# Performance work log

Measured on AMD Instinct MI355X. Metric: run time of the kernel, lower is better.

## Reference

```python
import jax, jax.numpy as jnp
import numpy as np

N_ROW = 50000
N_COL = 50000
E = 600000
D = 128
NEG_SLOPE = 0.01  # torch LeakyReLU default


def _leaky(x):
    return jnp.where(x >= 0, x, NEG_SLOPE * x)


def _mlp(x, W1, b1, W2, b2):
    # (Linear -> LeakyReLU) x2, matching nn.Sequential in Conv_layer
    h = _leaky(x @ W1 + b1)
    return _leaky(h @ W2 + b2)


def setup_inputs() -> dict:
    key = jax.random.key(0)
    ks = jax.random.split(key, 16)
    inp = {
        "feat_row": jax.random.normal(ks[0], (N_ROW, D), jnp.float32),
        "feat_col": jax.random.normal(ks[1], (N_COL, D), jnp.float32),
        "src_c2r": jax.random.randint(ks[2], (E,), 0, N_COL, jnp.int32),
        "dst_c2r": jax.random.randint(ks[3], (E,), 0, N_ROW, jnp.int32),
        "w_c2r": jax.random.uniform(ks[4], (E,), jnp.float32),
        "src_r2c": jax.random.randint(ks[5], (E,), 0, N_ROW, jnp.int32),
        "dst_r2c": jax.random.randint(ks[6], (E,), 0, N_COL, jnp.int32),
        "w_r2c": jax.random.uniform(ks[7], (E,), jnp.float32),
        "W1_c2r": jax.random.normal(ks[8], (D, D), jnp.float32) / np.sqrt(D),
        "b1_c2r": jax.random.normal(ks[9], (D,), jnp.float32) * 0.01,
        "W2_c2r": jax.random.normal(ks[10], (D, D), jnp.float32) / np.sqrt(D),
        "b2_c2r": jax.random.normal(ks[11], (D,), jnp.float32) * 0.01,
        "W1_r2c": jax.random.normal(ks[12], (D, D), jnp.float32) / np.sqrt(D),
        "b1_r2c": jax.random.normal(ks[13], (D,), jnp.float32) * 0.01,
        "W2_r2c": jax.random.normal(ks[14], (D, D), jnp.float32) / np.sqrt(D),
        "b2_r2c": jax.random.normal(ks[15], (D,), jnp.float32) * 0.01,
        "eps_c2r": jnp.zeros((), jnp.float32),  # DGL GINConv init_eps=0
        "eps_r2c": jnp.zeros((), jnp.float32),
    }
    return inp


def reference(feat_row, feat_col, src_c2r, dst_c2r, w_c2r, src_r2c, dst_r2c, w_r2c,
              W1_c2r, b1_c2r, W2_c2r, b2_c2r, W1_r2c, b1_r2c, W2_r2c, b2_r2c,
              eps_c2r, eps_r2c):
    # col -> row GINConv (edge-weighted sum aggregation)
    msg = feat_col[src_c2r] * w_c2r[:, None]                       # [E, D]
    agg_row = jax.ops.segment_sum(msg, dst_c2r, num_segments=N_ROW)
    h_row = _mlp((1.0 + eps_c2r) * feat_row + agg_row, W1_c2r, b1_c2r, W2_c2r, b2_c2r)
    # row -> col GINConv using updated row features
    msg2 = h_row[src_r2c] * w_r2c[:, None]                         # [E, D]
    agg_col = jax.ops.segment_sum(msg2, dst_r2c, num_segments=N_COL)
    h_col = _mlp((1.0 + eps_r2c) * feat_col + agg_col, W1_r2c, b1_r2c, W2_r2c, b2_r2c)
    # residual (use_residual=True): add pre-conv embeddings
    return h_row + feat_row, h_col + feat_col
```

## Files before the change

### kernel.cpp

```cpp
#include <hip/hip_runtime.h>
#include <hip/hip_bf16.h>

#define NROW 50000
#define NCOL 50000
#define DDIM 128
#define CAP  32

typedef __bf16 bf16_t;
typedef __bf16 bf16x2 __attribute__((ext_vector_type(2)));
typedef __bf16 bf16x8 __attribute__((ext_vector_type(8)));
typedef float  f32x4  __attribute__((ext_vector_type(4)));

__device__ __forceinline__ float lrelu(float v) { return v >= 0.f ? v : 0.01f * v; }

__device__ __forceinline__ float ldf(const void* p, size_t i, bool f) {
    return f ? ((const float*)p)[i] : (float)((const bf16_t*)p)[i];
}

__device__ __forceinline__ bool dtf(const int* flags, int fi) {
    return (fi == -1) ? true : (fi == -2) ? false : (flags[fi] != 0);
}

struct TensorTab { const void* p[18]; int n[18]; };

// ... 19 lines not shown
        unsigned low = w & 0xffffu;
        if (low) {
            int e = (int)((low >> 7) & 0xffu);
            if (e >= 90 && e <= 141) atomicAdd(&vb, 1);
            else                     atomicAdd(&vf, 1);
        }
    }
    __syncthreads();
    if (tid == 0) flags[t] = (isFloatArr && vf > vb) ? 1 : 0;
}

__device__ __forceinline__ void fill_edges(
    int e, const int* __restrict__ dst, const int* __restrict__ srcArr,
    const void* __restrict__ wArr, int nE, int* __restrict__ counts,
    int2* __restrict__ slots2, int* __restrict__ ovCnt,
    int* __restrict__ ovList, bool fW)
{
    if (e >= nE) return;
    int d = dst[e];
    int pos = atomicAdd(&counts[d], 1);
    if (pos < CAP) {
        int2 pk;
        pk.x = srcArr[e];
        pk.y = __float_as_int(ldf(wArr, e, fW));
        slots2[(size_t)d * CAP + pos] = pk;
    } else {
        int k = atomicAdd(ovCnt, 1);
        ovList[k] = e;
    }
}

struct WPtrs { const void* W[4]; int fi[4]; };

__global__ __launch_bounds__(256) void prep_fill(
    WPtrs P, const int* __restrict__ flags, __bf16* __restrict__ wfp,
    const void* __restrict__ feat, __bf16* __restrict__ cbuf, int n8,
    int fiFeat, int cblocks,
    const int* __restrict__ f_dst, const int* __restrict__ f_src,
    const void* __restrict__ f_w, int f_nE, int* __restrict__ f_counts,
    int2* __restrict__ f_slots2, int* __restrict__ f_ovCnt,
    int* __restrict__ f_ovList, int f_fiW)
{
    const int b = blockIdx.x;
    const int tid = threadIdx.x;
    if (b < cblocks) {
        int i = b * 256 + tid;
        if (i >= n8) return;
        const bool f = dtf(flags, fiFeat);
        bf16x8 v;
        if (f) {
            f32x4 a = ((const f32x4*)feat)[i * 2];
            f32x4 c = ((const f32x4*)feat)[i * 2 + 1];
#pragma unroll
            for (int j = 0; j < 4; ++j) { v[j] = (__bf16)a[j]; v[j + 4] = (__bf16)c[j]; }
        } else {
            v = ((const bf16x8*)feat)[i];
        }
        ((bf16x8*)cbuf)[i] = v;
    } else if (b < cblocks + 32) {
        int slot = (b - cblocks) * 256 + tid;
        if (slot >= 4 * 2048) return;
        int m = slot >> 11, sIdx = slot & 2047;
        bool f = flags[P.fi[m]] != 0;
        int l = sIdx & 63, combo = sIdx >> 6;
        int ct = combo >> 2, kk = combo & 3;
        int col  = ct * 16 + (l & 15);
        int krow = kk * 32 + (l >> 4) * 8;
        bf16x8 v;
#pragma unroll
        for (int j = 0; j < 8; ++j)
            v[j] = (__bf16)ldf(P.W[m], (size_t)(krow + j) * DDIM + col, f);
        ((bf16x8*)wfp)[slot] = v;
    } else {
        int e = (b - cblocks - 32) * 256 + tid;
        fill_edges(e, f_dst, f_src, f_w, f_nE, f_counts, f_slots2,
                   f_ovCnt, f_ovList, dtf(flags, f_fiW));
    }
}

__global__ __launch_bounds__(256) void segsum_scan(
    const __bf16* __restrict__ gsrc, const int* __restrict__ counts,
    const int2* __restrict__ slots2, float* __restrict__ agg, int nRows,
    const int* __restrict__ srcArr, const int* __restrict__ dstArr,
    const void* __restrict__ wArr, const int* __restrict__ ovList,
    const int* __restrict__ ovCount, const int* __restrict__ flags, int fiW)
{
    int row = blockIdx.x * 4 + (threadIdx.x >> 6);
    if (row >= nRows) return;
    int lane = threadIdx.x & 63;

    int cntRaw = counts[row];
    int cnt = cntRaw > CAP ? CAP : cntRaw;

    int sr = 0; float wv = 0.f;
    if (lane < cnt) {
        int2 pk = slots2[(size_t)row * CAP + lane];
        sr = pk.x;
        wv = __int_as_float(pk.y);
    }

    float2* ap = (float2*)(agg + (size_t)row * DDIM) + lane;
    float2 acc0 = {0.f, 0.f}, acc1 = {0.f, 0.f};

    const bf16x2* fb = (const bf16x2*)gsrc;
    int i = 0;
// ... 159 lines not shown
    for (int cp = 0; cp < 2; ++cp) {
        const int ct = cp ? ct1 : ct0;
        f32x4 acc = {0.f, 0.f, 0.f, 0.f};
#pragma unroll
        for (int kk = 0; kk < 4; ++kk)
            acc = __builtin_amdgcn_mfma_f32_16x16x32_bf16(
                a2[kk], cp ? wfb[kk] : wfa[kk], acc, 0, 0, 0);
        float bias = cp ? b2b : b2a;
#pragma unroll
        for (int gg = 0; gg < 4; ++gg) {
            int row = rowBase + quad * 4 + gg;
            float v = lrelu(acc[gg] + bias);
            if (HOUT)
                At[(quad * 4 + gg) * 136 + ct * 16 + r] = (__bf16)v;
            if (row < N) {
                int col = ct * 16 + r;
                if (RESIDUAL) v += ldf(feat, (size_t)row * DDIM + col, fF);
                out[(size_t)row * DDIM + col] = v;
            }
        }
    }

    if (HOUT) {
        __syncthreads();
        int row = tid >> 4;
        int k0  = (tid & 15) * 8;
        int g   = rowBase + row;
        if (g < N)
            *(bf16x8*)&hout[(size_t)g * DDIM + k0] =
                *(const bf16x8*)&At[row * 136 + k0];
    }
}

__global__ __launch_bounds__(256) void prep_all(
    WPtrs P, const int* __restrict__ flags, __bf16* __restrict__ wfp,
    const void* __restrict__ feat, __bf16* __restrict__ cbuf, int n8, int fiFeat,
    int* __restrict__ zc, int zn, int cblocks, int zblocks)
{
    const int b = blockIdx.x;
    const int tid = threadIdx.x;
    if (b < cblocks) {
        int i = b * 256 + tid;
        if (i >= n8) return;
        const bool f = dtf(flags, fiFeat);
        bf16x8 v;
        if (f) {
            f32x4 a = ((const f32x4*)feat)[i * 2];
            f32x4 c = ((const f32x4*)feat)[i * 2 + 1];
#pragma unroll
            for (int j = 0; j < 4; ++j) { v[j] = (__bf16)a[j]; v[j + 4] = (__bf16)c[j]; }
        } else {
            v = ((const bf16x8*)feat)[i];
        }
        ((bf16x8*)cbuf)[i] = v;
    } else if (b < cblocks + zblocks) {
        int i = (b - cblocks) * 256 + tid;
        if (i < zn) zc[i] = 0;
    } else {
        int slot = (b - cblocks - zblocks) * 256 + tid;
        if (slot >= 4 * 2048) return;
        int m = slot >> 11, sIdx = slot & 2047;
        bool f = flags[P.fi[m]] != 0;
        int l = sIdx & 63, combo = sIdx >> 6;
        int ct = combo >> 2, kk = combo & 3;
        int col  = ct * 16 + (l & 15);
        int krow = kk * 32 + (l >> 4) * 8;
        bf16x8 v;
#pragma unroll
        for (int j = 0; j < 8; ++j)
            v[j] = (__bf16)ldf(P.W[m], (size_t)(krow + j) * DDIM + col, f);
        ((bf16x8*)wfp)[slot] = v;
    }
}

__global__ __launch_bounds__(256) void fill_slots_packed(
    const int* __restrict__ dst, const int* __restrict__ srcArr,
    const void* __restrict__ wArr, int nE, int* __restrict__ counts,
    int2* __restrict__ slots2, int* __restrict__ ovCount,
    int* __restrict__ ovList, float* __restrict__ agg,
    const int* __restrict__ flags, int fiW)
{
    int e = blockIdx.x * 256 + threadIdx.x;
    if (e >= nE) return;
    const bool fW = dtf(flags, fiW);
    int d = dst[e];
    int pos = atomicAdd(&counts[d], 1);
    if (pos < CAP) {
        int2 pk;
        pk.x = srcArr[e];
        pk.y = __float_as_int(ldf(wArr, e, fW));
        slots2[(size_t)d * CAP + pos] = pk;
    } else {
        if (pos == CAP) {
            f32x4 z = {0.f, 0.f, 0.f, 0.f};
            f32x4* rp = (f32x4*)(agg + (size_t)d * DDIM);
#pragma unroll 4
            for (int c = 0; c < DDIM / 4; ++c) rp[c] = z;
        }
        int k = atomicAdd(ovCount, 1);
        ovList[k] = e;
    }
}

__global__ __launch_bounds__(256) void segsum_ov(
    const __bf16* __restrict__ gsrc, const int* __restrict__ counts,
    const int2* __restrict__ slots2, float* __restrict__ agg, int nRows,
    const int* __restrict__ srcArr, const int* __restrict__ dstArr,
    const void* __restrict__ wArr, const int* __restrict__ ovList,
    const int* __restrict__ ovCount, const int* __restrict__ flags, int fiW,
    int gblocks)
{
    const int tid  = threadIdx.x;
    const int lane = tid & 63;

    if ((int)blockIdx.x >= gblocks) {
        const bool fW = dtf(flags, fiW);
        const int nOv = *ovCount;
        const int wv_ = tid >> 6;
        const int nWaves = 64 * 4;
        for (int k = (blockIdx.x - gblocks) * 4 + wv_; k < nOv; k += nWaves) {
            int e = ovList[k];
            int s = srcArr[e], d = dstArr[e];
            float wf = ldf(wArr, e, fW);
            bf16x2 v = ((const bf16x2*)gsrc)[(size_t)s * 64 + lane];
            float* ap = agg + (size_t)d * DDIM + lane * 2;
            unsafeAtomicAdd(ap + 0, (float)v[0] * wf);
            unsafeAtomicAdd(ap + 1, (float)v[1] * wf);
        }
        return;
    }

    int row = blockIdx.x * 4 + (tid >> 6);
    if (row >= nRows) return;

    int cntRaw = counts[row];
    int cnt = cntRaw > CAP ? CAP : cntRaw;

    int sr = 0; float wv = 0.f;
    if (lane < cnt) {
        int2 pk = slots2[(size_t)row * CAP + lane];
        sr = pk.x;
        wv = __int_as_float(pk.y);
    }

    float2* ap = (float2*)(agg + (size_t)row * DDIM) + lane;
    float2 acc0 = {0.f, 0.f}, acc1 = {0.f, 0.f};

    const bf16x2* fb = (const bf16x2*)gsrc;
    int i = 0;
    for (; i + 4 <= cnt; i += 4) {
        int   a0 = __shfl(sr, i),     a1 = __shfl(sr, i + 1);
        int   a2 = __shfl(sr, i + 2), a3 = __shfl(sr, i + 3);
        float w0 = __shfl(wv, i),     w1 = __shfl(wv, i + 1);
        float w2 = __shfl(wv, i + 2), w3 = __shfl(wv, i + 3);
        bf16x2 v0 = fb[(size_t)a0 * 64 + lane];
        bf16x2 v1 = fb[(size_t)a1 * 64 + lane];
        bf16x2 v2 = fb[(size_t)a2 * 64 + lane];
        bf16x2 v3 = fb[(size_t)a3 * 64 + lane];
        acc0.x += (float)v0[0] * w0; acc0.y += (float)v0[1] * w0;
        acc1.x += (float)v1[0] * w1; acc1.y += (float)v1[1] * w1;
        acc0.x += (float)v2[0] * w2; acc0.y += (float)v2[1] * w2;
        acc1.x += (float)v3[0] * w3; acc1.y += (float)v3[1] * w3;
    }
    for (; i < cnt; ++i) {
        int   a0 = __shfl(sr, i);
        float w0 = __shfl(wv, i);
        bf16x2 v0 = fb[(size_t)a0 * 64 + lane];
        acc0.x += (float)v0[0] * w0; acc0.y += (float)v0[1] * w0;
    }
    acc0.x += acc1.x; acc0.y += acc1.y;
    if (cntRaw > CAP) {
        unsafeAtomicAdd(&ap->x, acc0.x);
        unsafeAtomicAdd(&ap->y, acc0.y);
    } else {
        *ap = acc0;
    }
}

template <bool RESIDUAL, bool HOUT>
__global__ __launch_bounds__(256) void mlp_reg(
    const void* __restrict__ feat, const float* __restrict__ agg,
    const void* __restrict__ b1, const void* __restrict__ b2,
    const void* __restrict__ epsp, float* __restrict__ out, int N,
    const int* __restrict__ flags, int fiFeat, int fiB1, int fiB2, int fiEps,
    const __bf16* __restrict__ pW1, const __bf16* __restrict__ pW2,
    __bf16* __restrict__ hout, int* __restrict__ zc, int zn)
{
    __shared__ alignas(16) __bf16 h1t[64 * 136];

    const int tid  = threadIdx.x;
    if (zc) {
        int gi = blockIdx.x * 256 + tid;
        if (gi < zn) zc[gi] = 0;
    }

    const bool fF  = flags[fiFeat] != 0;
    const bool fB1 = flags[fiB1] != 0;
    const bool fB2 = flags[fiB2] != 0;
    const bool fE  = flags[fiEps] != 0;

    const int lane = tid & 63;
    const int wave = tid >> 6;
    const int quad = lane >> 4;
    const int r    = lane & 15;
    const int rowBase = blockIdx.x * 64 + wave * 16;

    const bf16x8* pw1v = (const bf16x8*)pW1;
    bf16x8 w1f[32];
#pragma unroll
    for (int i = 0; i < 32; ++i) w1f[i] = pw1v[i * 64 + lane];

    float bias1[8];
#pragma unroll
    for (int ct = 0; ct < 8; ++ct) bias1[ct] = ldf(b1, ct * 16 + r, fB1);
    const float eps1 = 1.f + ldf(epsp, 0, fE);

    bf16x8 a[4];
    {
        int rowA = rowBase + r;
        if (rowA < N) {
            size_t fb = (size_t)rowA * DDIM + quad * 8;
            const f32x4* gp = (const f32x4*)(agg + fb);
            if (fF) {
                const f32x4* fp = (const f32x4*)((const float*)feat + fb);
#pragma unroll
                for (int kk = 0; kk < 4; ++kk) {
                    f32x4 f0 = fp[kk * 8], f1 = fp[kk * 8 + 1];
                    f32x4 g0 = gp[kk * 8], g1 = gp[kk * 8 + 1];
                    bf16x8 av;
#pragma unroll
                    for (int j = 0; j < 4; ++j) {
                        av[j]     = (__bf16)(f0[j] * eps1 + g0[j]);
                        av[j + 4] = (__bf16)(f1[j] * eps1 + g1[j]);
                    }
                    a[kk] = av;
                }
            } else {
                const bf16x8* fp = (const bf16x8*)((const bf16_t*)feat + fb);
#pragma unroll
                for (int kk = 0; kk < 4; ++kk) {
                    bf16x8 fv = fp[kk * 4];
                    f32x4 g0 = gp[kk * 8], g1 = gp[kk * 8 + 1];
                    bf16x8 av;
#pragma unroll
                    for (int j = 0; j < 4; ++j) {
                        av[j]     = (__bf16)((float)fv[j]     * eps1 + g0[j]);
                        av[j + 4] = (__bf16)((float)fv[j + 4] * eps1 + g1[j]);
                    }
                    a[kk] = av;
                }
            }
        } else {
#pragma unroll
            for (int kk = 0; kk < 4; ++kk)
#pragma unroll
                for (int j = 0; j < 8; ++j) a[kk][j] = (__bf16)0.f;
        }
    }

#pragma unroll
    for (int ct = 0; ct < 8; ++ct) {
        f32x4 acc = {0.f, 0.f, 0.f, 0.f};
#pragma unroll
        for (int kk = 0; kk < 4; ++kk)
            acc = __builtin_amdgcn_mfma_f32_16x16x32_bf16(
                a[kk], w1f[ct * 4 + kk], acc, 0, 0, 0);
#pragma unroll
        for (int gg = 0; gg < 4; ++gg)
            h1t[(wave * 16 + quad * 4 + gg) * 136 + ct * 16 + r] =
                (__bf16)lrelu(acc[gg] + bias1[ct]);
    }

    bf16x8 a2[4];
#pragma unroll
    for (int kk = 0; kk < 4; ++kk)
        a2[kk] = *(const bf16x8*)&h1t[(wave * 16 + r) * 136 + kk * 32 + quad * 8];

    const bf16x8* pw2v = (const bf16x8*)pW2;
    bf16x8 w2f[32];
#pragma unroll
    for (int i = 0; i < 32; ++i) w2f[i] = pw2v[i * 64 + lane];
    float bias2[8];
#pragma unroll
    for (int ct = 0; ct < 8; ++ct) bias2[ct] = ldf(b2, ct * 16 + r, fB2);

#pragma unroll
    for (int ct = 0; ct < 8; ++ct) {
        f32x4 acc = {0.f, 0.f, 0.f, 0.f};
#pragma unroll
        for (int kk = 0; kk < 4; ++kk)
            acc = __builtin_amdgcn_mfma_f32_16x16x32_bf16(
                a2[kk], w2f[ct * 4 + kk], acc, 0, 0, 0);
#pragma unroll
        for (int gg = 0; gg < 4; ++gg) {
            int row = rowBase + quad * 4 + gg;
            float v = lrelu(acc[gg] + bias2[ct]);
            if (HOUT)
                h1t[(wave * 16 + quad * 4 + gg) * 136 + ct * 16 + r] = (__bf16)v;
            if (row < N) {
                int col = ct * 16 + r;
                if (RESIDUAL) v += ldf(feat, (size_t)row * DDIM + col, fF);
                out[(size_t)row * DDIM + col] = v;
            }
        }
    }

    if (HOUT) {
        __syncthreads();
        const int blockBase = blockIdx.x * 64;
#pragma unroll
        for (int c = 0; c < 4; ++c) {
            int chunk = tid + c * 256;
            int row = chunk >> 4;
            int k   = (chunk & 15) * 8;
            if (blockBase + row < N) {
                bf16x8 v = *(const bf16x8*)&h1t[row * 136 + k];
                *(bf16x8*)&hout[(size_t)(blockBase + row) * DDIM + k] = v;
            }
        }
    }
}

__global__ __launch_bounds__(256) void scatter_any(
    const void* __restrict__ feat, const int* __restrict__ src,
    const int* __restrict__ dst, const void* __restrict__ w,
    float* __restrict__ agg, int nE,
    const int* __restrict__ flags, int fiFeat, int fiW)
{
    const bool fF = dtf(flags, fiFeat);
    const bool fW = dtf(flags, fiW);
    int g = blockIdx.x * 256 + threadIdx.x;
    int e = g >> 5;
    if (e >= nE) return;
    int c = (g & 31) << 2;
    int s = src[e], d = dst[e];
    float wf = ldf(w, e, fW);
    size_t base = (size_t)s * DDIM + c;
    float* ap = agg + (size_t)d * DDIM + c;
    unsafeAtomicAdd(ap + 0, ldf(feat, base + 0, fF) * wf);
    unsafeAtomicAdd(ap + 1, ldf(feat, base + 1, fF) * wf);
    unsafeAtomicAdd(ap + 2, ldf(feat, base + 2, fF) * wf);
    unsafeAtomicAdd(ap + 3, ldf(feat, base + 3, fF) * wf);
}

__global__ __launch_bounds__(256) void residual_add(
    float* __restrict__ out, const void* __restrict__ feat, int n4,
    const int* __restrict__ flags, int fiFeat)
{
    const bool fF = flags[fiFeat] != 0;
    int i = blockIdx.x * 256 + threadIdx.x;
    if (i >= n4) return;
    f32x4 o = ((const f32x4*)out)[i];
    f32x4 r;
#pragma unroll
    for (int j = 0; j < 4; ++j) r[j] = o[j] + ldf(feat, (size_t)i * 4 + j, fF);
// ... 119 lines not shown
    for (int ct = 0; ct < 8; ++ct) {
        f32x4 acc = {0.f, 0.f, 0.f, 0.f};
#pragma unroll
        for (int kk = 0; kk < 4; ++kk)
            acc = __builtin_amdgcn_mfma_f32_16x16x32_bf16(
                a2[kk], wv[(ct * 4 + kk) * 64 + lane], acc, 0, 0, 0);
        float bias = ldf(b2, ct * 16 + r, fB2);
#pragma unroll
        for (int gg = 0; gg < 4; ++gg) {
            int row = rowBase + quad * 4 + gg;
            if (row < N) {
                int col = ct * 16 + r;
                float v = lrelu(acc[gg] + bias);
                if (RESIDUAL) v += ldf(feat, (size_t)row * DDIM + col, fF);
                out[(size_t)row * DDIM + col] = v;
            }
        }
    }
}

extern "C" void kernel_launch(void* const* d_in, const int* in_sizes, int n_in,
                              void* d_out, int out_size, void* d_ws, size_t ws_size,
                              hipStream_t stream)
{
    const int* src_c2r = (const int*)d_in[2];
    const int* dst_c2r = (const int*)d_in[3];
    const int* src_r2c = (const int*)d_in[5];
    const int* dst_r2c = (const int*)d_in[6];
    const int nE = in_sizes[2];

    char* wsb = (char*)d_ws;
    int*    flags  = (int*)wsb;
    __bf16* wfprep = (__bf16*)(wsb + 128);
    int*    countsA = (int*)(wsb + 128 + 131072);
    int*    ovCntA  = countsA + NROW;
    int*    countsB = countsA + NROW + 8;
    int*    ovCntB  = countsA + 2 * NROW + 8;
    size_t  ofsA2   = 128 + 131072 + ((size_t)2 * NROW + 16) * 4;
    ofsA2 = (ofsA2 + 15) & ~(size_t)15;
    int2*   slots2A2  = (int2*)(wsb + ofsA2);
    size_t  ofsOvA2   = ofsA2 + (size_t)NROW * CAP * 8;
    int*    ovListA2  = (int*)(wsb + ofsOvA2);
    int*    ovListB2  = ovListA2 + nE;
    size_t  ofsCbA2   = (ofsOvA2 + (size_t)nE * 8 + 15) & ~(size_t)15;
    __bf16* cbufA2    = (__bf16*)(wsb + ofsCbA2);
    const size_t NEED_A2 = ofsCbA2 + (size_t)NROW * DDIM * 2;

    int*    counts = (int*)(wsb + 128 + 131072);
    int*    ovCnt  = counts + NROW;
    size_t  ofs    = 128 + 131072 + ((size_t)NROW + 8) * 4;
    ofs = (ofs + 15) & ~(size_t)15;
    int2*   slots2 = (int2*)(wsb + ofs);
    size_t  ofsOvA = ofs + (size_t)NROW * CAP * 8;
    int*    ovListA = (int*)(wsb + ofsOvA);
    size_t  ofsCb  = (ofsOvA + (size_t)nE * 4 + 15) & ~(size_t)15;
    __bf16* cbuf   = (__bf16*)(wsb + ofsCb);
    const size_t NEED_A = ofsCb + (size_t)NROW * DDIM * 2;

    const bool tierA2 = ws_size >= NEED_A2;
    const bool tierA  = ws_size >= NEED_A;

    TensorTab T;
    for (int i = 0; i < 18; ++i) { T.p[i] = d_in[i]; T.n[i] = in_sizes[i]; }

    float* out_row = (float*)d_out;
    float* out_col = out_row + (size_t)NROW * DDIM;
    const size_t aggBytes = (size_t)NROW * DDIM * sizeof(float);

    const int eblocks  = (nE + 255) / 256;
    const int sblocks  = (nE * 32 + 255) / 256;
    const int mblocksR = (NROW + 63) / 64;
    const int mblocksC = (NCOL + 63) / 64;
    const int csR      = (NROW + 15) / 16;
    const int csC      = (NCOL + 15) / 16;
    const int gblocksR = (NROW + 3) / 4;
    const int gblocksC = (NCOL + 3) / 4;
    const int cblocks  = (NCOL * DDIM / 8 + 255) / 256;

    WPtrs P;
    P.W[0] = d_in[8];  P.fi[0] = 8;
    P.W[1] = d_in[10]; P.fi[1] = 10;
    P.W[2] = d_in[12]; P.fi[2] = 12;
    P.W[3] = d_in[14]; P.fi[3] = 14;

    if (tierA2) {
        const int zn2 = 2 * NROW + 16;
        const int zb2 = (zn2 + 255) / 256;
        detect_zero<<<18 + zb2, 256, 0, stream>>>(T, flags, countsA, zn2);
        prep_fill<<<cblocks + 32 + eblocks, 256, 0, stream>>>(
            P, flags, wfprep, d_in[1], cbufA2, NCOL * DDIM / 8, 1, cblocks,
            dst_c2r, src_c2r, d_in[4], nE, countsA, slots2A2, ovCntA,
            ovListA2, 4);
        segsum_scan<<<gblocksR, 256, 0, stream>>>(cbufA2, countsA, slots2A2,
            out_col, NROW, src_c2r, dst_c2r, d_in[4], ovListA2, ovCntA,
            flags, 4);
        mlp_cs<true, true><<<csR + eblocks, 256, 0, stream>>>(
            d_in[0], out_col, d_in[9], d_in[11], d_in[16],
            out_row, NROW, flags, 0, 9, 11, 16,
            wfprep + 0 * 16384, wfprep + 1 * 16384, cbufA2,
            csR, dst_r2c, src_r2c, d_in[7], nE, countsB, slots2A2,
            ovCntB, ovListB2, 7);
        segsum_scan<<<gblocksC, 256, 0, stream>>>(cbufA2, countsB, slots2A2,
            out_col, NCOL, src_r2c, dst_r2c, d_in[7], ovListB2, ovCntB,
            flags, 7);
        mlp_cs<true, false><<<csC, 256, 0, stream>>>(
            d_in[1], out_col, d_in[13], d_in[15], d_in[17],
            out_col, NCOL, flags, 1, 13, 15, 17,
            wfprep + 2 * 16384, wfprep + 3 * 16384, nullptr,
            csC, nullptr, nullptr, nullptr, 0, nullptr, nullptr,
            nullptr, nullptr, 0);
    } else if (tierA) {
        const int zblocks = ((NROW + 8) + 255) / 256;
        const int zn      = NROW + 8;
        detect_zero<<<18, 256, 0, stream>>>(T, flags, nullptr, 0);
        prep_all<<<cblocks + zblocks + 32, 256, 0, stream>>>(
            P, flags, wfprep, d_in[1], cbuf, NCOL * DDIM / 8, 1,
            counts, zn, cblocks, zblocks);
        fill_slots_packed<<<eblocks, 256, 0, stream>>>(dst_c2r, src_c2r,
            d_in[4], nE, counts, slots2, ovCnt, ovListA, out_col, flags, 4);
        segsum_ov<<<gblocksR + 64, 256, 0, stream>>>(cbuf, counts, slots2,
            out_col, NROW, src_c2r, dst_c2r, d_in[4], ovListA, ovCnt,
            flags, 4, gblocksR);
        mlp_reg<true, true><<<mblocksR, 256, 0, stream>>>(
            d_in[0], out_col, d_in[9], d_in[11], d_in[16],
            out_row, NROW, flags, 0, 9, 11, 16,
            wfprep + 0 * 16384, wfprep + 1 * 16384, cbuf, counts, zn);
        fill_slots_packed<<<eblocks, 256, 0, stream>>>(dst_r2c, src_r2c,
            d_in[7], nE, counts, slots2, ovCnt, ovListA, out_col, flags, 7);
        segsum_ov<<<gblocksC + 64, 256, 0, stream>>>(cbuf, counts, slots2,
            out_col, NCOL, src_r2c, dst_r2c, d_in[7], ovListA, ovCnt,
            flags, 7, gblocksC);
        mlp_reg<true, false><<<mblocksC, 256, 0, stream>>>(
            d_in[1], out_col, d_in[13], d_in[15], d_in[17],
            out_col, NCOL, flags, 1, 13, 15, 17,
            wfprep + 2 * 16384, wfprep + 3 * 16384, nullptr, nullptr, 0);
    } else {
        detect_zero<<<18, 256, 0, stream>>>(T, flags, nullptr, 0);
        hipMemsetAsync(out_col, 0, aggBytes, stream);
        scatter_any<<<sblocks, 256, 0, stream>>>(d_in[1], src_c2r, dst_c2r,
            d_in[4], out_col, nE, flags, 1, 4);
        mlp_kernel<false><<<mblocksR, 256, 0, stream>>>(
            d_in[0], out_col, d_in[8], d_in[9], d_in[10], d_in[11], d_in[16],
            out_row, NROW, flags, 0, 8, 9, 10, 11, 16);

        hipMemsetAsync(out_col, 0, aggBytes, stream);
        scatter_any<<<sblocks, 256, 0, stream>>>(out_row, src_r2c, dst_r2c,
            d_in[7], out_col, nE, flags, -1, 7);
        residual_add<<<(NROW * DDIM / 4 + 255) / 256, 256, 0, stream>>>(
            out_row, d_in[0], NROW * DDIM / 4, flags, 0);
        mlp_kernel<true><<<mblocksC, 256, 0, stream>>>(
            d_in[1], out_col, d_in[12], d_in[13], d_in[14], d_in[15], d_in[17],
            out_col, NCOL, flags, 1, 12, 13, 14, 15, 17);
    }
}
```

Before: 309.5 us.

## Fuse gather-sum into MLP kernel and interleave edge-fill with compute blocks

```diff
diff --git a/kernel.cpp b/kernel.cpp
--- a/kernel.cpp
+++ b/kernel.cpp
@@ -75,6 +75,276 @@
 
 struct WPtrs { const void* W[4]; int fi[4]; };
 
+__device__ __forceinline__ void prep_one(WPtrs P, const int* flags,
+                                         __bf16* wfp, int slot)
+{
+    if (slot >= 4 * 2048) return;
+    int m = slot >> 11, sIdx = slot & 2047;
+    bool f = flags[P.fi[m]] != 0;
+    int l = sIdx & 63, combo = sIdx >> 6;
+    int ct = combo >> 2, kk = combo & 3;
+    int col  = ct * 16 + (l & 15);
+    int krow = kk * 32 + (l >> 4) * 8;
+    bf16x8 v;
+#pragma unroll
+    for (int j = 0; j < 8; ++j)
+        v[j] = (__bf16)ldf(P.W[m], (size_t)(krow + j) * DDIM + col, f);
+    ((bf16x8*)wfp)[slot] = v;
+}
+
+__device__ __forceinline__ void convert_one(const void* __restrict__ feat,
+                                            __bf16* __restrict__ cbuf,
+                                            int i, int n8, bool f)
+{
+    if (i >= n8) return;
+    bf16x8 v;
+    if (f) {
+        f32x4 a = ((const f32x4*)feat)[i * 2];
+        f32x4 c = ((const f32x4*)feat)[i * 2 + 1];
+#pragma unroll
+        for (int j = 0; j < 4; ++j) { v[j] = (__bf16)a[j]; v[j + 4] = (__bf16)c[j]; }
+    } else {
+        v = ((const bf16x8*)feat)[i];
+    }
+    ((bf16x8*)cbuf)[i] = v;
+}
+
+__global__ __launch_bounds__(256) void prep_fill_i(
+    WPtrs P, const int* __restrict__ flags, __bf16* __restrict__ wfp,
+    const void* __restrict__ feat, __bf16* __restrict__ cbuf, int n8,
+    int fiFeat, int cb, int eb, int K7,
+    const int* __restrict__ f_dst, const int* __restrict__ f_src,
+    const void* __restrict__ f_w, int f_nE, int* __restrict__ f_counts,
+    int2* __restrict__ f_slots2, int* __restrict__ f_ovCnt,
+    int* __restrict__ f_ovList, int f_fiW)
+{
+    const int g = blockIdx.x;
+    const int tid = threadIdx.x;
+    if (g >= K7) {
+        prep_one(P, flags, wfp, (g - K7) * 256 + tid);
+        return;
+    }
+    int grp = g / 7, rem = g % 7;
+    if (rem < 4) {
+        int b = grp * 4 + rem;
+        if (b >= cb) return;
+        convert_one(feat, cbuf, b * 256 + tid, n8, dtf(flags, fiFeat));
+    } else {
+        int b = grp * 3 + (rem - 4);
+        if (b >= eb) return;
+        fill_edges(b * 256 + tid, f_dst, f_src, f_w, f_nE, f_counts,
+                   f_slots2, f_ovCnt, f_ovList, dtf(flags, f_fiW));
+    }
+}
+
+template <bool RESIDUAL, bool HOUT>
+__global__ __launch_bounds__(256) void mlp_fused(
+    const __bf16* __restrict__ gsrc, const int* __restrict__ counts,
+    const int2* __restrict__ slots2, const int* __restrict__ srcArr,
+    const int* __restrict__ dstArr, const void* __restrict__ wArr,
+    const int* __restrict__ ovList, const int* __restrict__ ovCount, int fiW,
+    const void* __restrict__ feat, const void* __restrict__ b1,
+    const void* __restrict__ b2, const void* __restrict__ epsp,
+    float* __restrict__ out, int N, const int* __restrict__ flags,
+    int fiFeat, int fiB1, int fiB2, int fiEps,
+    const __bf16* __restrict__ pW1, const __bf16* __restrict__ pW2,
+    __bf16* __restrict__ hout,
+    int mlpBlocks, int fillBlocks,
+    const int* __restrict__ f_dst, const int* __restrict__ f_src,
+    const void* __restrict__ f_w, int f_nE, int* __restrict__ f_counts,
+    int2* __restrict__ f_slots2, int* __restrict__ f_ovCnt,
+    int* __restrict__ f_ovList, int f_fiW)
+{
+    __shared__ alignas(16) __bf16 At[16 * 136];
+    __shared__ alignas(16) __bf16 H1[16 * 136];
+
+    const int tid = threadIdx.x;
+    int bid;
+    if (f_dst) {
+        int grp = (int)blockIdx.x / 7, rem = (int)blockIdx.x % 7;
+        if (rem >= 4) {
+            int b = grp * 3 + (rem - 4);
+            if (b < fillBlocks)
+                fill_edges(b * 256 + tid, f_dst, f_src, f_w, f_nE, f_counts,
+                           f_slots2, f_ovCnt, f_ovList, dtf(flags, f_fiW));
+            return;
+        }
+        bid = grp * 4 + rem;
+        if (bid >= mlpBlocks) return;
+    } else {
+        bid = blockIdx.x;
+        if (bid >= mlpBlocks) return;
+    }
+
+    const bool fF  = flags[fiFeat] != 0;
+    const bool fB1 = flags[fiB1] != 0;
+    const bool fB2 = flags[fiB2] != 0;
+    const bool fE  = flags[fiEps] != 0;
+
+    const int lane = tid & 63;
+    const int wave = tid >> 6;
+    const int quad = lane >> 4;
+    const int r    = lane & 15;
+    const int rowBase = bid * 16;
+    const float eps1 = 1.f + ldf(epsp, 0, fE);
+
+    {
+        const bf16x2* fb = (const bf16x2*)gsrc;
+        for (int j = 0; j < 4; ++j) {
+            int lrow = wave * 4 + j;
+            int row  = rowBase + lrow;
+            bf16x2 o;
+            if (row < N) {
+                int cntRaw = counts[row];
+                int cnt = cntRaw > CAP ? CAP : cntRaw;
+                int sr = 0; float wv = 0.f;
+                if (lane < cnt) {
+                    int2 pk = slots2[(size_t)row * CAP + lane];
+                    sr = pk.x;
+                    wv = __int_as_float(pk.y);
+                }
+                float2 acc0 = {0.f, 0.f}, acc1 = {0.f, 0.f};
+                int i = 0;
+                for (; i + 4 <= cnt; i += 4) {
+                    int   a0 = __shfl(sr, i),     a1 = __shfl(sr, i + 1);
+                    int   a2 = __shfl(sr, i + 2), a3 = __shfl(sr, i + 3);
+                    float w0 = __shfl(wv, i),     w1 = __shfl(wv, i + 1);
+                    float w2 = __shfl(wv, i + 2), w3 = __shfl(wv, i + 3);
+                    bf16x2 v0 = fb[(size_t)a0 * 64 + lane];
+                    bf16x2 v1 = fb[(size_t)a1 * 64 + lane];
+                    bf16x2 v2 = fb[(size_t)a2 * 64 + lane];
+                    bf16x2 v3 = fb[(size_t)a3 * 64 + lane];
+                    acc0.x += (float)v0[0] * w0; acc0.y += (float)v0[1] * w0;
+                    acc1.x += (float)v1[0] * w1; acc1.y += (float)v1[1] * w1;
+                    acc0.x += (float)v2[0] * w2; acc0.y += (float)v2[1] * w2;
+                    acc1.x += (float)v3[0] * w3; acc1.y += (float)v3[1] * w3;
+                }
+                for (; i < cnt; ++i) {
+                    int   a0 = __shfl(sr, i);
+                    float w0 = __shfl(wv, i);
+                    bf16x2 v0 = fb[(size_t)a0 * 64 + lane];
+                    acc0.x += (float)v0[0] * w0; acc0.y += (float)v0[1] * w0;
+                }
+                if (cntRaw > CAP) {
+                    const bool fW = dtf(flags, fiW);
+                    int nOv = *ovCount;
+                    for (int k = 0; k < nOv; ++k) {
+                        int e = ovList[k];
+                        if (dstArr[e] == row) {
+                            int s = srcArr[e];
+                            float wf = ldf(wArr, e, fW);
+                            bf16x2 v = fb[(size_t)s * 64 + lane];
+                            acc0.x += (float)v[0] * wf;
+                            acc0.y += (float)v[1] * wf;
+                        }
+                    }
+                }
+                float ax = acc0.x + acc1.x, ay = acc0.y + acc1.y;
+                float f0, f1;
+                if (fF) {
+                    float2 fv = ((const float2*)((const float*)feat +
+                                 (size_t)row * DDIM))[lane];
+                    f0 = fv.x; f1 = fv.y;
+                } else {
+                    bf16x2 fv = ((const bf16x2*)((const bf16_t*)feat +
+                                 (size_t)row * DDIM))[lane];
+                    f0 = (float)fv[0]; f1 = (float)fv[1];
+                }
+                o[0] = (__bf16)(f0 * eps1 + ax);
+                o[1] = (__bf16)(f1 * eps1 + ay);
+            } else {
+                o[0] = (__bf16)0.f; o[1] = (__bf16)0.f;
+            }
+            *(bf16x2*)&At[lrow * 136 + lane * 2] = o;
+        }
+    }
+    __syncthreads();
+
+    bf16x8 a[4];
+#pragma unroll
+    for (int kk = 0; kk < 4; ++kk)
+        a[kk] = *(const bf16x8*)&At[r * 136 + kk * 32 + quad * 8];
+
+    const int ct0 = wave * 2, ct1 = ct0 + 1;
+
+    const bf16x8* pw1v = (const bf16x8*)pW1;
+    bf16x8 wfa[4], wfb[4];
+#pragma unroll
+    for (int kk = 0; kk < 4; ++kk) {
+        wfa[kk] = pw1v[(ct0 * 4 + kk) * 64 + lane];
+        wfb[kk] = pw1v[(ct1 * 4 + kk) * 64 + lane];
+    }
+    float b1a = ldf(b1, ct0 * 16 + r, fB1);
+    float b1b = ldf(b1, ct1 * 16 + r, fB1);
+
+    {
+        f32x4 acc = {0.f, 0.f, 0.f, 0.f};
+#pragma unroll
+        for (int kk = 0; kk < 4; ++kk)
+            acc = __builtin_amdgcn_mfma_f32_16x16x32_bf16(a[kk], wfa[kk], acc, 0, 0, 0);
+#pragma unroll
+        for (int gg = 0; gg < 4; ++gg)
+            H1[(quad * 4 + gg) * 136 + ct0 * 16 + r] = (__bf16)lrelu(acc[gg] + b1a);
+    }
+    {
+        f32x4 acc = {0.f, 0.f, 0.f, 0.f};
+#pragma unroll
+        for (int kk = 0; kk < 4; ++kk)
+            acc = __builtin_amdgcn_mfma_f32_16x16x32_bf16(a[kk], wfb[kk], acc, 0, 0, 0);
+#pragma unroll
+        for (int gg = 0; gg < 4; ++gg)
+            H1[(quad * 4 + gg) * 136 + ct1 * 16 + r] = (__bf16)lrelu(acc[gg] + b1b);
+    }
+    __syncthreads();
+
+    bf16x8 a2[4];
+#pragma unroll
+    for (int kk = 0; kk < 4; ++kk)
+        a2[kk] = *(const bf16x8*)&H1[r * 136 + kk * 32 + quad * 8];
+
+    const bf16x8* pw2v = (const bf16x8*)pW2;
+#pragma unroll
+    for (int kk = 0; kk < 4; ++kk) {
+        wfa[kk] = pw2v[(ct0 * 4 + kk) * 64 + lane];
+        wfb[kk] = pw2v[(ct1 * 4 + kk) * 64 + lane];
+    }
+    float b2a = ldf(b2, ct0 * 16 + r, fB2);
+    float b2b = ldf(b2, ct1 * 16 + r, fB2);
+
+#pragma unroll
+    for (int cp = 0; cp < 2; ++cp) {
+        const int ct = cp ? ct1 : ct0;
+        f32x4 acc = {0.f, 0.f, 0.f, 0.f};
+#pragma unroll
+        for (int kk = 0; kk < 4; ++kk)
+            acc = __builtin_amdgcn_mfma_f32_16x16x32_bf16(
+                a2[kk], cp ? wfb[kk] : wfa[kk], acc, 0, 0, 0);
+        float bias = cp ? b2b : b2a;
+#pragma unroll
+        for (int gg = 0; gg < 4; ++gg) {
+            int row = rowBase + quad * 4 + gg;
+            float v = lrelu(acc[gg] + bias);
+            if (HOUT)
+                At[(quad * 4 + gg) * 136 + ct * 16 + r] = (__bf16)v;
+            if (row < N) {
+                int col = ct * 16 + r;
+                if (RESIDUAL) v += ldf(feat, (size_t)row * DDIM + col, fF);
+                out[(size_t)row * DDIM + col] = v;
+            }
+        }
+    }
+
+    if (HOUT) {
+        __syncthreads();
+        int row = tid >> 4;
+        int k0  = (tid & 15) * 8;
+        int g   = rowBase + row;
+        if (g < N)
+            *(bf16x8*)&hout[(size_t)g * DDIM + k0] =
+                *(const bf16x8*)&At[row * 136 + k0];
+    }
+}
+
 __global__ __launch_bounds__(256) void prep_fill(
     WPtrs P, const int* __restrict__ flags, __bf16* __restrict__ wfp,
     const void* __restrict__ feat, __bf16* __restrict__ cbuf, int n8,
@@ -87,33 +357,9 @@
     const int b = blockIdx.x;
     const int tid = threadIdx.x;
     if (b < cblocks) {
-        int i = b * 256 + tid;
-        if (i >= n8) return;
-        const bool f = dtf(flags, fiFeat);
-        bf16x8 v;
-        if (f) {
-            f32x4 a = ((const f32x4*)feat)[i * 2];
-            f32x4 c = ((const f32x4*)feat)[i * 2 + 1];
-#pragma unroll
-            for (int j = 0; j < 4; ++j) { v[j] = (__bf16)a[j]; v[j + 4] = (__bf16)c[j]; }
-        } else {
-            v = ((const bf16x8*)feat)[i];
-        }
-        ((bf16x8*)cbuf)[i] = v;
+        convert_one(feat, cbuf, b * 256 + tid, n8, dtf(flags, fiFeat));
     } else if (b < cblocks + 32) {
-        int slot = (b - cblocks) * 256 + tid;
-        if (slot >= 4 * 2048) return;
-        int m = slot >> 11, sIdx = slot & 2047;
-        bool f = flags[P.fi[m]] != 0;
-        int l = sIdx & 63, combo = sIdx >> 6;
-        int ct = combo >> 2, kk = combo & 3;
-        int col  = ct * 16 + (l & 15);
-        int krow = kk * 32 + (l >> 4) * 8;
-        bf16x8 v;
-#pragma unroll
-        for (int j = 0; j < 8; ++j)
-            v[j] = (__bf16)ldf(P.W[m], (size_t)(krow + j) * DDIM + col, f);
-        ((bf16x8*)wfp)[slot] = v;
+        prep_one(P, flags, wfp, (b - cblocks) * 256 + tid);
     } else {
         int e = (b - cblocks - 32) * 256 + tid;
         fill_edges(e, f_dst, f_src, f_w, f_nE, f_counts, f_slots2,
@@ -339,295 +585,6 @@
     }
 }
 
-__global__ __launch_bounds__(256) void prep_all(
-    WPtrs P, const int* __restrict__ flags, __bf16* __restrict__ wfp,
-    const void* __restrict__ feat, __bf16* __restrict__ cbuf, int n8, int fiFeat,
-    int* __restrict__ zc, int zn, int cblocks, int zblocks)
-{
-    const int b = blockIdx.x;
-    const int tid = threadIdx.x;
-    if (b < cblocks) {
-        int i = b * 256 + tid;
-        if (i >= n8) return;
-        const bool f = dtf(flags, fiFeat);
-        bf16x8 v;
-        if (f) {
-            f32x4 a = ((const f32x4*)feat)[i * 2];
-            f32x4 c = ((const f32x4*)feat)[i * 2 + 1];
-#pragma unroll
-            for (int j = 0; j < 4; ++j) { v[j] = (__bf16)a[j]; v[j + 4] = (__bf16)c[j]; }
-        } else {
-            v = ((const bf16x8*)feat)[i];
-        }
-        ((bf16x8*)cbuf)[i] = v;
-    } else if (b < cblocks + zblocks) {
-        int i = (b - cblocks) * 256 + tid;
-        if (i < zn) zc[i] = 0;
-    } else {
-        int slot = (b - cblocks - zblocks) * 256 + tid;
-        if (slot >= 4 * 2048) return;
-        int m = slot >> 11, sIdx = slot & 2047;
-        bool f = flags[P.fi[m]] != 0;
-        int l = sIdx & 63, combo = sIdx >> 6;
-        int ct = combo >> 2, kk = combo & 3;
-        int col  = ct * 16 + (l & 15);
-        int krow = kk * 32 + (l >> 4) * 8;
-        bf16x8 v;
-#pragma unroll
-        for (int j = 0; j < 8; ++j)
-            v[j] = (__bf16)ldf(P.W[m], (size_t)(krow + j) * DDIM + col, f);
-        ((bf16x8*)wfp)[slot] = v;
-    }
-}
-
-__global__ __launch_bounds__(256) void fill_slots_packed(
-    const int* __restrict__ dst, const int* __restrict__ srcArr,
-    const void* __restrict__ wArr, int nE, int* __restrict__ counts,
-    int2* __restrict__ slots2, int* __restrict__ ovCount,
-    int* __restrict__ ovList, float* __restrict__ agg,
-    const int* __restrict__ flags, int fiW)
-{
-    int e = blockIdx.x * 256 + threadIdx.x;
-    if (e >= nE) return;
-    const bool fW = dtf(flags, fiW);
-    int d = dst[e];
-    int pos = atomicAdd(&counts[d], 1);
-    if (pos < CAP) {
-        int2 pk;
-        pk.x = srcArr[e];
-        pk.y = __float_as_int(ldf(wArr, e, fW));
-        slots2[(size_t)d * CAP + pos] = pk;
-    } else {
-        if (pos == CAP) {
-            f32x4 z = {0.f, 0.f, 0.f, 0.f};
-            f32x4* rp = (f32x4*)(agg + (size_t)d * DDIM);
-#pragma unroll 4
-            for (int c = 0; c < DDIM / 4; ++c) rp[c] = z;
-        }
-        int k = atomicAdd(ovCount, 1);
-        ovList[k] = e;
-    }
-}
-
-__global__ __launch_bounds__(256) void segsum_ov(
-    const __bf16* __restrict__ gsrc, const int* __restrict__ counts,
-    const int2* __restrict__ slots2, float* __restrict__ agg, int nRows,
-    const int* __restrict__ srcArr, const int* __restrict__ dstArr,
-    const void* __restrict__ wArr, const int* __restrict__ ovList,
-    const int* __restrict__ ovCount, const int* __restrict__ flags, int fiW,
-    int gblocks)
-{
-    const int tid  = threadIdx.x;
-    const int lane = tid & 63;
-
-    if ((int)blockIdx.x >= gblocks) {
-        const bool fW = dtf(flags, fiW);
-        const int nOv = *ovCount;
-        const int wv_ = tid >> 6;
-        const int nWaves = 64 * 4;
-        for (int k = (blockIdx.x - gblocks) * 4 + wv_; k < nOv; k += nWaves) {
-            int e = ovList[k];
-            int s = srcArr[e], d = dstArr[e];
-            float wf = ldf(wArr, e, fW);
-            bf16x2 v = ((const bf16x2*)gsrc)[(size_t)s * 64 + lane];
-            float* ap = agg + (size_t)d * DDIM + lane * 2;
-            unsafeAtomicAdd(ap + 0, (float)v[0] * wf);
-            unsafeAtomicAdd(ap + 1, (float)v[1] * wf);
-        }
-        return;
-    }
-
-    int row = blockIdx.x * 4 + (tid >> 6);
-    if (row >= nRows) return;
-
-    int cntRaw = counts[row];
-    int cnt = cntRaw > CAP ? CAP : cntRaw;
-
-    int sr = 0; float wv = 0.f;
-    if (lane < cnt) {
-        int2 pk = slots2[(size_t)row * CAP + lane];
-        sr = pk.x;
-        wv = __int_as_float(pk.y);
-    }
-
-    float2* ap = (float2*)(agg + (size_t)row * DDIM) + lane;
-    float2 acc0 = {0.f, 0.f}, acc1 = {0.f, 0.f};
-
-    const bf16x2* fb = (const bf16x2*)gsrc;
-    int i = 0;
-    for (; i + 4 <= cnt; i += 4) {
-        int   a0 = __shfl(sr, i),     a1 = __shfl(sr, i + 1);
-        int   a2 = __shfl(sr, i + 2), a3 = __shfl(sr, i + 3);
-        float w0 = __shfl(wv, i),     w1 = __shfl(wv, i + 1);
-        float w2 = __shfl(wv, i + 2), w3 = __shfl(wv, i + 3);
-        bf16x2 v0 = fb[(size_t)a0 * 64 + lane];
-        bf16x2 v1 = fb[(size_t)a1 * 64 + lane];
-        bf16x2 v2 = fb[(size_t)a2 * 64 + lane];
-        bf16x2 v3 = fb[(size_t)a3 * 64 + lane];
-        acc0.x += (float)v0[0] * w0; acc0.y += (float)v0[1] * w0;
-        acc1.x += (float)v1[0] * w1; acc1.y += (float)v1[1] * w1;
-        acc0.x += (float)v2[0] * w2; acc0.y += (float)v2[1] * w2;
-        acc1.x += (float)v3[0] * w3; acc1.y += (float)v3[1] * w3;
-    }
-    for (; i < cnt; ++i) {
-        int   a0 = __shfl(sr, i);
-        float w0 = __shfl(wv, i);
-        bf16x2 v0 = fb[(size_t)a0 * 64 + lane];
-        acc0.x += (float)v0[0] * w0; acc0.y += (float)v0[1] * w0;
-    }
-    acc0.x += acc1.x; acc0.y += acc1.y;
-    if (cntRaw > CAP) {
-        unsafeAtomicAdd(&ap->x, acc0.x);
-        unsafeAtomicAdd(&ap->y, acc0.y);
-    } else {
-        *ap = acc0;
-    }
-}
-
-template <bool RESIDUAL, bool HOUT>
-__global__ __launch_bounds__(256) void mlp_reg(
-    const void* __restrict__ feat, const float* __restrict__ agg,
-    const void* __restrict__ b1, const void* __restrict__ b2,
-    const void* __restrict__ epsp, float* __restrict__ out, int N,
-    const int* __restrict__ flags, int fiFeat, int fiB1, int fiB2, int fiEps,
-    const __bf16* __restrict__ pW1, const __bf16* __restrict__ pW2,
-    __bf16* __restrict__ hout, int* __restrict__ zc, int zn)
-{
-    __shared__ alignas(16) __bf16 h1t[64 * 136];
-
-    const int tid  = threadIdx.x;
-    if (zc) {
-        int gi = blockIdx.x * 256 + tid;
-        if (gi < zn) zc[gi] = 0;
-    }
-
-    const bool fF  = flags[fiFeat] != 0;
-    const bool fB1 = flags[fiB1] != 0;
-    const bool fB2 = flags[fiB2] != 0;
-    const bool fE  = flags[fiEps] != 0;
-
-    const int lane = tid & 63;
-    const int wave = tid >> 6;
-    const int quad = lane >> 4;
-    const int r    = lane & 15;
-    const int rowBase = blockIdx.x * 64 + wave * 16;
-
-    const bf16x8* pw1v = (const bf16x8*)pW1;
-    bf16x8 w1f[32];
-#pragma unroll
-    for (int i = 0; i < 32; ++i) w1f[i] = pw1v[i * 64 + lane];
-
-    float bias1[8];
-#pragma unroll
-    for (int ct = 0; ct < 8; ++ct) bias1[ct] = ldf(b1, ct * 16 + r, fB1);
-    const float eps1 = 1.f + ldf(epsp, 0, fE);
-
-    bf16x8 a[4];
-    {
-        int rowA = rowBase + r;
-        if (rowA < N) {
-            size_t fb = (size_t)rowA * DDIM + quad * 8;
-            const f32x4* gp = (const f32x4*)(agg + fb);
-            if (fF) {
-                const f32x4* fp = (const f32x4*)((const float*)feat + fb);
-#pragma unroll
-                for (int kk = 0; kk < 4; ++kk) {
-                    f32x4 f0 = fp[kk * 8], f1 = fp[kk * 8 + 1];
-                    f32x4 g0 = gp[kk * 8], g1 = gp[kk * 8 + 1];
-                    bf16x8 av;
-#pragma unroll
-                    for (int j = 0; j < 4; ++j) {
-                        av[j]     = (__bf16)(f0[j] * eps1 + g0[j]);
-                        av[j + 4] = (__bf16)(f1[j] * eps1 + g1[j]);
-                    }
-                    a[kk] = av;
-                }
-            } else {
-                const bf16x8* fp = (const bf16x8*)((const bf16_t*)feat + fb);
-#pragma unroll
-                for (int kk = 0; kk < 4; ++kk) {
-                    bf16x8 fv = fp[kk * 4];
-                    f32x4 g0 = gp[kk * 8], g1 = gp[kk * 8 + 1];
-                    bf16x8 av;
-#pragma unroll
-                    for (int j = 0; j < 4; ++j) {
-                        av[j]     = (__bf16)((float)fv[j]     * eps1 + g0[j]);
-                        av[j + 4] = (__bf16)((float)fv[j + 4] * eps1 + g1[j]);
-                    }
-                    a[kk] = av;
-                }
-            }
-        } else {
-#pragma unroll
-            for (int kk = 0; kk < 4; ++kk)
-#pragma unroll
-                for (int j = 0; j < 8; ++j) a[kk][j] = (__bf16)0.f;
-        }
-    }
-
-#pragma unroll
-    for (int ct = 0; ct < 8; ++ct) {
-        f32x4 acc = {0.f, 0.f, 0.f, 0.f};
-#pragma unroll
-        for (int kk = 0; kk < 4; ++kk)
-            acc = __builtin_amdgcn_mfma_f32_16x16x32_bf16(
-                a[kk], w1f[ct * 4 + kk], acc, 0, 0, 0);
-#pragma unroll
-        for (int gg = 0; gg < 4; ++gg)
-            h1t[(wave * 16 + quad * 4 + gg) * 136 + ct * 16 + r] =
-                (__bf16)lrelu(acc[gg] + bias1[ct]);
-    }
-
-    bf16x8 a2[4];
-#pragma unroll
-    for (int kk = 0; kk < 4; ++kk)
-        a2[kk] = *(const bf16x8*)&h1t[(wave * 16 + r) * 136 + kk * 32 + quad * 8];
-
-    const bf16x8* pw2v = (const bf16x8*)pW2;
-    bf16x8 w2f[32];
-#pragma unroll
-    for (int i = 0; i < 32; ++i) w2f[i] = pw2v[i * 64 + lane];
-    float bias2[8];
-#pragma unroll
-    for (int ct = 0; ct < 8; ++ct) bias2[ct] = ldf(b2, ct * 16 + r, fB2);
-
-#pragma unroll
-    for (int ct = 0; ct < 8; ++ct) {
-        f32x4 acc = {0.f, 0.f, 0.f, 0.f};
-#pragma unroll
-        for (int kk = 0; kk < 4; ++kk)
-            acc = __builtin_amdgcn_mfma_f32_16x16x32_bf16(
-                a2[kk], w2f[ct * 4 + kk], acc, 0, 0, 0);
-#pragma unroll
-        for (int gg = 0; gg < 4; ++gg) {
-            int row = rowBase + quad * 4 + gg;
-            float v = lrelu(acc[gg] + bias2[ct]);
-            if (HOUT)
-                h1t[(wave * 16 + quad * 4 + gg) * 136 + ct * 16 + r] = (__bf16)v;
-            if (row < N) {
-                int col = ct * 16 + r;
-                if (RESIDUAL) v += ldf(feat, (size_t)row * DDIM + col, fF);
-                out[(size_t)row * DDIM + col] = v;
-            }
-        }
-    }
-
-    if (HOUT) {
-        __syncthreads();
-        const int blockBase = blockIdx.x * 64;
-#pragma unroll
-        for (int c = 0; c < 4; ++c) {
-            int chunk = tid + c * 256;
-            int row = chunk >> 4;
-            int k   = (chunk & 15) * 8;
-            if (blockBase + row < N) {
-                bf16x8 v = *(const bf16x8*)&h1t[row * 136 + k];
-                *(bf16x8*)&hout[(size_t)(blockBase + row) * DDIM + k] = v;
-            }
-        }
-    }
-}
-
 __global__ __launch_bounds__(256) void scatter_any(
     const void* __restrict__ feat, const int* __restrict__ src,
     const int* __restrict__ dst, const void* __restrict__ w,
@@ -813,10 +770,22 @@
     char* wsb = (char*)d_ws;
     int*    flags  = (int*)wsb;
     __bf16* wfprep = (__bf16*)(wsb + 128);
-    int*    countsA = (int*)(wsb + 128 + 131072);
-    int*    ovCntA  = countsA + NROW;
-    int*    countsB = countsA + NROW + 8;
-    int*    ovCntB  = countsA + 2 * NROW + 8;
+
+    int*    cntA   = (int*)(wsb + 128 + 131072);
+    int*    ovCntA = cntA + NROW;
+    int*    cntB   = cntA + NROW + 8;
+    int*    ovCntB = cntA + 2 * NROW + 8;
+    size_t  o3 = 128 + 131072 + ((size_t)2 * NROW + 16) * 4;
+    o3 = (o3 + 15) & ~(size_t)15;
+    int2*   sl2A = (int2*)(wsb + o3);  o3 += (size_t)NROW * CAP * 8;
+    int2*   sl2B = (int2*)(wsb + o3);  o3 += (size_t)NROW * CAP * 8;
+    int*    ovLA = (int*)(wsb + o3);   o3 += (size_t)nE * 4;
+    int*    ovLB = (int*)(wsb + o3);   o3 += (size_t)nE * 4;
+    o3 = (o3 + 15) & ~(size_t)15;
+    __bf16* cbX  = (__bf16*)(wsb + o3); o3 += (size_t)NCOL * DDIM * 2;
+    __bf16* cbH  = (__bf16*)(wsb + o3); o3 += (size_t)NROW * DDIM * 2;
+    const size_t NEED_A3 = o3;
+
     size_t  ofsA2   = 128 + 131072 + ((size_t)2 * NROW + 16) * 4;
     ofsA2 = (ofsA2 + 15) & ~(size_t)15;
     int2*   slots2A2  = (int2*)(wsb + ofsA2);
@@ -827,19 +796,8 @@
     __bf16* cbufA2    = (__bf16*)(wsb + ofsCbA2);
     const size_t NEED_A2 = ofsCbA2 + (size_t)NROW * DDIM * 2;
 
-    int*    counts = (int*)(wsb + 128 + 131072);
-    int*    ovCnt  = counts + NROW;
-    size_t  ofs    = 128 + 131072 + ((size_t)NROW + 8) * 4;
-    ofs = (ofs + 15) & ~(size_t)15;
-    int2*   slots2 = (int2*)(wsb + ofs);
-    size_t  ofsOvA = ofs + (size_t)NROW * CAP * 8;
-    int*    ovListA = (int*)(wsb + ofsOvA);
-    size_t  ofsCb  = (ofsOvA + (size_t)nE * 4 + 15) & ~(size_t)15;
-    __bf16* cbuf   = (__bf16*)(wsb + ofsCb);
-    const size_t NEED_A = ofsCb + (size_t)NROW * DDIM * 2;
-
+    const bool tierA3 = ws_size >= NEED_A3;
     const bool tierA2 = ws_size >= NEED_A2;
-    const bool tierA  = ws_size >= NEED_A;
 
     TensorTab T;
     for (int i = 0; i < 18; ++i) { T.p[i] = d_in[i]; T.n[i] = in_sizes[i]; }
@@ -857,6 +815,8 @@
     const int gblocksR = (NROW + 3) / 4;
     const int gblocksC = (NCOL + 3) / 4;
     const int cblocks  = (NCOL * DDIM / 8 + 255) / 256;
+    const int zn2      = 2 * NROW + 16;
+    const int zb2      = (zn2 + 255) / 256;
 
     WPtrs P;
     P.W[0] = d_in[8];  P.fi[0] = 8;
@@ -864,24 +824,50 @@
     P.W[2] = d_in[12]; P.fi[2] = 12;
     P.W[3] = d_in[14]; P.fi[3] = 14;
 
-    if (tierA2) {
-        const int zn2 = 2 * NROW + 16;
-        const int zb2 = (zn2 + 255) / 256;
-        detect_zero<<<18 + zb2, 256, 0, stream>>>(T, flags, countsA, zn2);
+    if (tierA3) {
+        detect_zero<<<18 + zb2, 256, 0, stream>>>(T, flags, cntA, zn2);
+        {
+            int ka = (cblocks + 3) / 4, kb = (eblocks + 2) / 3;
+            int K = ka > kb ? ka : kb;
+            prep_fill_i<<<7 * K + 32, 256, 0, stream>>>(
+                P, flags, wfprep, d_in[1], cbX, NCOL * DDIM / 8, 1,
+                cblocks, eblocks, 7 * K,
+                dst_c2r, src_c2r, d_in[4], nE, cntA, sl2A, ovCntA, ovLA, 4);
+        }
+        {
+            int ka = (csR + 3) / 4, kb = (eblocks + 2) / 3;
+            int K = ka > kb ? ka : kb;
+            mlp_fused<true, true><<<7 * K, 256, 0, stream>>>(
+                cbX, cntA, sl2A, src_c2r, dst_c2r, d_in[4], ovLA, ovCntA, 4,
+                d_in[0], d_in[9], d_in[11], d_in[16],
+                out_row, NROW, flags, 0, 9, 11, 16,
+                wfprep + 0 * 16384, wfprep + 1 * 16384, cbH,
+                csR, eblocks, dst_r2c, src_r2c, d_in[7], nE, cntB, sl2B,
+                ovCntB, ovLB, 7);
+        }
+        mlp_fused<true, false><<<csC, 256, 0, stream>>>(
+            cbH, cntB, sl2B, src_r2c, dst_r2c, d_in[7], ovLB, ovCntB, 7,
+            d_in[1], d_in[13], d_in[15], d_in[17],
+            out_col, NCOL, flags, 1, 13, 15, 17,
+            wfprep + 2 * 16384, wfprep + 3 * 16384, nullptr,
+            csC, 0, nullptr, nullptr, nullptr, 0, nullptr, nullptr,
+            nullptr, nullptr, 0);
+    } else if (tierA2) {
+        detect_zero<<<18 + zb2, 256, 0, stream>>>(T, flags, cntA, zn2);
         prep_fill<<<cblocks + 32 + eblocks, 256, 0, stream>>>(
             P, flags, wfprep, d_in[1], cbufA2, NCOL * DDIM / 8, 1, cblocks,
-            dst_c2r, src_c2r, d_in[4], nE, countsA, slots2A2, ovCntA,
+            dst_c2r, src_c2r, d_in[4], nE, cntA, slots2A2, ovCntA,
             ovListA2, 4);
-        segsum_scan<<<gblocksR, 256, 0, stream>>>(cbufA2, countsA, slots2A2,
+        segsum_scan<<<gblocksR, 256, 0, stream>>>(cbufA2, cntA, slots2A2,
             out_col, NROW, src_c2r, dst_c2r, d_in[4], ovListA2, ovCntA,
             flags, 4);
         mlp_cs<true, true><<<csR + eblocks, 256, 0, stream>>>(
             d_in[0], out_col, d_in[9], d_in[11], d_in[16],
             out_row, NROW, flags, 0, 9, 11, 16,
             wfprep + 0 * 16384, wfprep + 1 * 16384, cbufA2,
-            csR, dst_r2c, src_r2c, d_in[7], nE, countsB, slots2A2,
+            csR, dst_r2c, src_r2c, d_in[7], nE, cntB, slots2A2,
             ovCntB, ovListB2, 7);
-        segsum_scan<<<gblocksC, 256, 0, stream>>>(cbufA2, countsB, slots2A2,
+        segsum_scan<<<gblocksC, 256, 0, stream>>>(cbufA2, cntB, slots2A2,
             out_col, NCOL, src_r2c, dst_r2c, d_in[7], ovListB2, ovCntB,
             flags, 7);
         mlp_cs<true, false><<<csC, 256, 0, stream>>>(
@@ -890,31 +876,6 @@
             wfprep + 2 * 16384, wfprep + 3 * 16384, nullptr,
             csC, nullptr, nullptr, nullptr, 0, nullptr, nullptr,
             nullptr, nullptr, 0);
-    } else if (tierA) {
-        const int zblocks = ((NROW + 8) + 255) / 256;
-        const int zn      = NROW + 8;
-        detect_zero<<<18, 256, 0, stream>>>(T, flags, nullptr, 0);
-        prep_all<<<cblocks + zblocks + 32, 256, 0, stream>>>(
-            P, flags, wfprep, d_in[1], cbuf, NCOL * DDIM / 8, 1,
-            counts, zn, cblocks, zblocks);
-        fill_slots_packed<<<eblocks, 256, 0, stream>>>(dst_c2r, src_c2r,
-            d_in[4], nE, counts, slots2, ovCnt, ovListA, out_col, flags, 4);
-        segsum_ov<<<gblocksR + 64, 256, 0, stream>>>(cbuf, counts, slots2,
-            out_col, NROW, src_c2r, dst_c2r, d_in[4], ovListA, ovCnt,
-            flags, 4, gblocksR);
-        mlp_reg<true, true><<<mblocksR, 256, 0, stream>>>(
-            d_in[0], out_col, d_in[9], d_in[11], d_in[16],
-            out_row, NROW, flags, 0, 9, 11, 16,
-            wfprep + 0 * 16384, wfprep + 1 * 16384, cbuf, counts, zn);
-        fill_slots_packed<<<eblocks, 256, 0, stream>>>(dst_r2c, src_r2c,
-            d_in[7], nE, counts, slots2, ovCnt, ovListA, out_col, flags, 7);
-        segsum_ov<<<gblocksC + 64, 256, 0, stream>>>(cbuf, counts, slots2,
-            out_col, NCOL, src_r2c, dst_r2c, d_in[7], ovListA, ovCnt,
-            flags, 7, gblocksC);
-        mlp_reg<true, false><<<mblocksC, 256, 0, stream>>>(
-            d_in[1], out_col, d_in[13], d_in[15], d_in[17],
-            out_col, NCOL, flags, 1, 13, 15, 17,
-            wfprep + 2 * 16384, wfprep + 3 * 16384, nullptr, nullptr, 0);
     } else {
         detect_zero<<<18, 256, 0, stream>>>(T, flags, nullptr, 0);
         hipMemsetAsync(out_col, 0, aggBytes, stream);
```

New measurement: 306.6 us. Within noise of the previous version (-0.9%).
